# Optimization experiments

Measured on AMD Instinct MI355X. Metric: run time of the kernel, lower is better.

Reference implementation:

```python
import jax, jax.numpy as jnp
import numpy as np

N_NODES = 100000
N_FEAT = 512
HIDDEN = 64
N_CLASS = 40
N_EDGES = 3200000


def setup_inputs() -> dict:
    key = jax.random.key(0)
    k1, k2, k3, k4, k5, k6 = jax.random.split(key, 6)
    x = jax.random.normal(k1, (N_NODES, N_FEAT), dtype=jnp.float32)
    edge_index = jax.random.randint(k2, (2, N_EDGES), 0, N_NODES, dtype=jnp.int64)
    # Glorot-style init like PyG GCNConv
    s1 = (6.0 / (N_FEAT + HIDDEN)) ** 0.5
    s2 = (6.0 / (HIDDEN + N_CLASS)) ** 0.5
    W1 = jax.random.uniform(k3, (N_FEAT, HIDDEN), jnp.float32, -s1, s1)
    b1 = jnp.zeros((HIDDEN,), jnp.float32)
    W2 = jax.random.uniform(k4, (HIDDEN, N_CLASS), jnp.float32, -s2, s2)
    b2 = jnp.zeros((N_CLASS,), jnp.float32)
    return {"x": x, "edge_index": edge_index, "W1": W1, "b1": b1, "W2": W2, "b2": b2}


def _gcn_norm(edge_index, n_nodes):
    # add self-loops, symmetric normalization (PyG gcn_norm defaults)
    loops = jnp.arange(n_nodes, dtype=edge_index.dtype)
    src = jnp.concatenate([edge_index[0], loops])
    dst = jnp.concatenate([edge_index[1], loops])
    deg = jax.ops.segment_sum(jnp.ones_like(dst, dtype=jnp.float32), dst,
                              num_segments=n_nodes)
    dinv = jnp.where(deg > 0, jax.lax.rsqrt(deg), 0.0)
    norm = dinv[src] * dinv[dst]  # [E + N]
    return src, dst, norm


def _gcn_conv(h, src, dst, norm, W, b, n_nodes):
    h = h @ W                                   # [N, out]
    msg = h[src] * norm[:, None]                # gather + scale, [E+N, out]
    out = jax.ops.segment_sum(msg, dst, num_segments=n_nodes)  # scatter-add
    return out + b


def reference(x, edge_index, W1, b1, W2, b2):
    n = x.shape[0]
    src, dst, norm = _gcn_norm(edge_index, n)
    h = _gcn_conv(x, src, dst, norm, W1, b1, n)
    h = jax.nn.relu(h)
    h = _gcn_conv(h, src, dst, norm, W2, b2, n)
    return jax.nn.softmax(h, axis=-1)
```

## Files before the change

kernel.cpp:

```cpp
#include <hip/hip_runtime.h>
#include <hip/hip_bf16.h>
#include <math.h>

#define NFEAT 512
#define HID   64
#define NCLS  40
#define T2STRIDE 64

#define BSHIFT 9
#define BSIZE  512
#define BCAP   20480
#define CHUNK  4096

typedef __attribute__((ext_vector_type(8))) short bf16x8v;
typedef __attribute__((ext_vector_type(4))) float f32x4v;

__device__ __forceinline__ float rl_f(float v, int l) {
    return __int_as_float(__builtin_amdgcn_readlane(__float_as_int(v), l));
}
__device__ __forceinline__ unsigned short f2bf(float f) {
    __hip_bfloat16 h = __float2bfloat16(f);
    return *(unsigned short*)&h;
}


__global__ __launch_bounds__(256) void bin_scatter(const int* __restrict__ ei, int e,
                                                   int nbuckets,
                                                   int* __restrict__ bucket_cursor,
                                                   int* __restrict__ stage) {
    __shared__ int packed_s[CHUNK];
    __shared__ unsigned char bkt_s[CHUNK];
    __shared__ int hist[256];
    __shared__ int base_s[256];
    __shared__ int lcur[256];
    int t = threadIdx.x;
    int b0 = blockIdx.x * CHUNK;
    int cnt = min(CHUNK, e - b0);
    for (int i = t; i < 256; i += 256) hist[i] = 0;
    __syncthreads();
    for (int i = t; i < cnt; i += 256) {
        int s = ei[b0 + i];
        int d = ei[e + b0 + i];
        packed_s[i] = (s << BSHIFT) | (d & (BSIZE - 1));
        bkt_s[i] = (unsigned char)(d >> BSHIFT);
        atomicAdd(&hist[d >> BSHIFT], 1);
    }
    __syncthreads();
    for (int i = t; i < nbuckets; i += 256) {
        int c = hist[i];
        base_s[i] = c ? atomicAdd(&bucket_cursor[i], c) : 0;
        lcur[i] = 0;
    }
    __syncthreads();
    for (int i = t; i < cnt; i += 256) {
        int bk = bkt_s[i];
        int pos = base_s[bk] + atomicAdd(&lcur[bk], 1);
        if (pos < BCAP) stage[(size_t)bk * BCAP + pos] = packed_s[i];
    }
}

__global__ __launch_bounds__(256) void bucket_csr(const int* __restrict__ stage,
                                                  const int* __restrict__ bucket_cursor,
                                                  int* __restrict__ row_ptr,
                                                  float* __restrict__ dinv,
                                                  int* __restrict__ col,
                                                  int n, int e, int nbuckets) {
    __shared__ int sc[256];
    __shared__ int hist[BSIZE];
    __shared__ int lbase[BSIZE];
    __shared__ int psum[256];
    int b = blockIdx.x;
    int t = threadIdx.x;
    int v = (t < nbuckets) ? bucket_cursor[t] : 0;
    sc[t] = v;
    __syncthreads();
    #pragma unroll
    for (int off = 1; off < 256; off <<= 1) {
        int u = (t >= off) ? sc[t - off] : 0;
        __syncthreads();
        sc[t] += u;
        __syncthreads();
    }
    int base0 = (b > 0) ? sc[b - 1] : 0;
    if (b == 0 && t == 0) row_ptr[n] = e;

    int cnt = min(bucket_cursor[b], BCAP);
    int node0 = b << BSHIFT;
    int nnodes = min(BSIZE, n - node0);
    const int* st = stage + (size_t)b * BCAP;
    for (int i = t; i < BSIZE; i += 256) hist[i] = 0;
    __syncthreads();
    for (int i = t; i < cnt; i += 256) atomicAdd(&hist[st[i] & (BSIZE - 1)], 1);
    __syncthreads();
    int h0 = hist[2 * t], h1 = hist[2 * t + 1];
    int pair = h0 + h1;
    psum[t] = pair;
    __syncthreads();
    #pragma unroll
    for (int off = 1; off < 256; off <<= 1) {
        int u = (t >= off) ? psum[t - off] : 0;
        __syncthreads();
        psum[t] += u;
        __syncthreads();
    }
    int ex = psum[t] - pair;
    lbase[2 * t] = ex;
    lbase[2 * t + 1] = ex + h0;
    __syncthreads();
    for (int i = t; i < nnodes; i += 256) {
        row_ptr[node0 + i] = base0 + lbase[i];
        dinv[node0 + i] = rsqrtf((float)(hist[i] + 1));
    }
    __syncthreads();
    for (int i = t; i < cnt; i += 256) {
        int p = st[i];
        int pos = atomicAdd(&lbase[p & (BSIZE - 1)], 1);
        col[base0 + pos] = ((unsigned)p) >> BSHIFT;
    }
}


__global__ __launch_bounds__(256) void w1_to_bf16t(const float* __restrict__ W1,
                                                   unsigned short* __restrict__ w1bt) {
    int idx = blockIdx.x * 256 + threadIdx.x;
    int c = idx >> 9, k = idx & 511;
    w1bt[idx] = f2bf(W1[k * HID + c]);
}


__global__ __launch_bounds__(256) void gemm1(const float* __restrict__ x,
                                             const unsigned short* __restrict__ w1bt,
                                             const float* __restrict__ dinv,
                                             __hip_bfloat16* __restrict__ t1, int n) {
    __shared__ __align__(16) unsigned short As[64][40];
    __shared__ __align__(16) unsigned short Bs[64][40];
    int t = threadIdx.x;
    int m0 = blockIdx.x * 64;
    int w = t >> 6, lane = t & 63;
    int lrow = lane & 15, lkg = lane >> 4;
    f32x4v acc[4] = {};

    int arow = t >> 2;
    int akg = t & 3;
    int grow = m0 + arow; if (grow >= n) grow = n - 1;
    const float* xrow = x + (size_t)grow * NFEAT;

    for (int k0 = 0; k0 < NFEAT; k0 += 32) {
        float4 v0 = *(const float4*)(xrow + k0 + akg * 8);
        float4 v1 = *(const float4*)(xrow + k0 + akg * 8 + 4);
        union { unsigned short u[8]; uint4 q; } P;
        P.u[0] = f2bf(v0.x); P.u[1] = f2bf(v0.y); P.u[2] = f2bf(v0.z); P.u[3] = f2bf(v0.w);
        P.u[4] = f2bf(v1.x); P.u[5] = f2bf(v1.y); P.u[6] = f2bf(v1.z); P.u[7] = f2bf(v1.w);
        *(uint4*)&As[arow][akg * 8] = P.q;
        *(uint4*)&Bs[arow][akg * 8] = *(const uint4*)(w1bt + arow * 512 + k0 + akg * 8);
        __syncthreads();
        bf16x8v af = *(const bf16x8v*)&As[w * 16 + lrow][lkg * 8];
        #pragma unroll
        for (int nb = 0; nb < 4; nb++) {
            bf16x8v bfv = *(const bf16x8v*)&Bs[nb * 16 + lrow][lkg * 8];
            acc[nb] = __builtin_amdgcn_mfma_f32_16x16x32_bf16(af, bfv, acc[nb], 0, 0, 0);
        }
        __syncthreads();
    }
    #pragma unroll
    for (int r = 0; r < 4; r++) {
        int row = m0 + w * 16 + lkg * 4 + r;
        if (row < n) {
            float d = dinv[row];
            #pragma unroll
            for (int nb = 0; nb < 4; nb++) {
                t1[(size_t)row * HID + nb * 16 + lrow] = __float2bfloat16(acc[nb][r] * d);
            }
        }
    }
}


#define UNPACK_ADD(pv) do { \
    acc[0] += __uint_as_float((pv).x << 16); acc[1] += __uint_as_float((pv).x & 0xffff0000u); \
    acc[2] += __uint_as_float((pv).y << 16); acc[3] += __uint_as_float((pv).y & 0xffff0000u); \
    acc[4] += __uint_as_float((pv).z << 16); acc[5] += __uint_as_float((pv).z & 0xffff0000u); \
    acc[6] += __uint_as_float((pv).w << 16); acc[7] += __uint_as_float((pv).w & 0xffff0000u); } while (0)

__global__ __launch_bounds__(256) void agg1_gemm2(const __hip_bfloat16* __restrict__ t1,
                                                  const int* __restrict__ row_ptr,
                                                  const int* __restrict__ col,
                                                  const float* __restrict__ dinv,
                                                  const float* __restrict__ b1,
                                                  const float* __restrict__ W2,
                                                  __hip_bfloat16* __restrict__ t2, int n) {
    __shared__ float2 w2p[32 * 40];
    for (int i = threadIdx.x; i < 32 * 40; i += 256) {
        int k2 = i / 40, c = i - k2 * 40;
        w2p[i] = make_float2(W2[(2 * k2) * 40 + c], W2[(2 * k2 + 1) * 40 + c]);
    }
    __syncthreads();

    int wave = threadIdx.x >> 6;
    int lane = threadIdx.x & 63;
    int node0 = blockIdx.x * 4 + wave;
    int node = (node0 < n) ? node0 : n - 1;
    int r = lane & 7;
    int slot = lane >> 3;

    const uint4* t1q = (const uint4*)t1;
    int s0 = row_ptr[node], s1 = row_ptr[node + 1];

    float acc[8] = {0.f, 0.f, 0.f, 0.f, 0.f, 0.f, 0.f, 0.f};

    if (lane < 8) {
        uint4 pv = t1q[(size_t)node * 8 + lane];
        UNPACK_ADD(pv);
    }

    int bpbase = slot * 4;
    for (int jb = s0; jb < s1; jb += 32) {
        int rem = s1 - jb;
        int ll = lane & 31;
        int cidx = col[jb + ((ll < rem) ? ll : 0)];
        int srcg[4];
        #pragma unroll
        for (int g = 0; g < 4; g++) {
            int src = __builtin_amdgcn_ds_bpermute(bpbase + 32 * g, cidx);
            srcg[g] = (8 * g + slot < rem) ? src : n;
        }
        uint4 pv[4];
        #pragma unroll
        for (int g = 0; g < 4; g++) pv[g] = t1q[(size_t)srcg[g] * 8 + r];
        #pragma unroll
        for (int g = 0; g < 4; g++) { UNPACK_ADD(pv[g]); }
    }

    #pragma unroll
    for (int off = 8; off < 64; off <<= 1) {
        #pragma unroll
        for (int j = 0; j < 8; j++) acc[j] += __shfl_xor(acc[j], off, 64);
    }

    float dn = dinv[node];
    const float4* b1q = (const float4*)b1;
    float4 ba = b1q[2 * r];
    float4 bb = b1q[2 * r + 1];
    float hv[8];
    hv[0] = fmaxf(0.f, dn * acc[0] + ba.x);
    hv[1] = fmaxf(0.f, dn * acc[1] + ba.y);
    hv[2] = fmaxf(0.f, dn * acc[2] + ba.z);
    hv[3] = fmaxf(0.f, dn * acc[3] + ba.w);
    hv[4] = fmaxf(0.f, dn * acc[4] + bb.x);
    hv[5] = fmaxf(0.f, dn * acc[5] + bb.y);
    hv[6] = fmaxf(0.f, dn * acc[6] + bb.z);
    hv[7] = fmaxf(0.f, dn * acc[7] + bb.w);

    int c = (lane < 40) ? lane : 39;
    float o = 0.0f;
    #pragma unroll
    for (int rr = 0; rr < 8; rr++) {
        #pragma unroll
        for (int j2 = 0; j2 < 4; j2++) {
            float ha = rl_f(hv[2 * j2],     rr);
            float hb = rl_f(hv[2 * j2 + 1], rr);
            float2 wv = w2p[(4 * rr + j2) * 40 + c];
            o += ha * wv.x + hb * wv.y;
        }
    }
    if (node0 < n && lane < 40)
        t2[(size_t)node * T2STRIDE + lane] = __float2bfloat16(dn * o);
}


__global__ __launch_bounds__(256) void agg2_softmax(const __hip_bfloat16* __restrict__ t2,
                                                    const int* __restrict__ row_ptr,
                                                    const int* __restrict__ col,
                                                    const float* __restrict__ dinv,
                                                    const float* __restrict__ b2,
                                                    float* __restrict__ out, int n) {
    int wave = threadIdx.x >> 6;
    int lane = threadIdx.x & 63;
    int node = blockIdx.x * 4 + wave;
    if (node >= n) return;
    int h = lane >> 5;
    int p = lane & 31;
    int pc = (p < 20) ? p : 19;
    const unsigned* t2d = (const unsigned*)t2;
    int s0 = row_ptr[node], s1 = row_ptr[node + 1];

    float ax = 0.f, ay = 0.f;
    if (h == 0) {
        unsigned v = t2d[(size_t)node * 32 + pc];
        ax = __uint_as_float(v << 16);
        ay = __uint_as_float(v & 0xffff0000u);
    }
    for (int jb = s0; jb < s1; jb += 16) {
        int rem = s1 - jb;
        int cv = col[jb + ((lane < rem) ? lane : 0)];
        int srcg[8];
        #pragma unroll
        for (int i = 0; i < 8; i++) {
            int eid = 2 * i + h;
            int src = __builtin_amdgcn_ds_bpermute(4 * eid, cv);
            srcg[i] = (eid < rem) ? src : n;
        }
        unsigned pv[8];
        #pragma unroll
        for (int i = 0; i < 8; i++) pv[i] = t2d[(size_t)srcg[i] * 32 + pc];
        #pragma unroll
        for (int i = 0; i < 8; i++) {
            ax += __uint_as_float(pv[i] << 16);
            ay += __uint_as_float(pv[i] & 0xffff0000u);
        }
    }
    ax += __shfl_xor(ax, 32, 64);
    ay += __shfl_xor(ay, 32, 64);

    float dn = dinv[node];
    float2 bv = *(const float2*)(b2 + 2 * pc);
    float lx = dn * ax + bv.x;
    float ly = dn * ay + bv.y;
    float m = (p < 20) ? fmaxf(lx, ly) : -INFINITY;
    #pragma unroll
    for (int off = 16; off; off >>= 1) m = fmaxf(m, __shfl_xor(m, off, 64));
    float ex = (p < 20) ? expf(lx - m) : 0.0f;
    float ey = (p < 20) ? expf(ly - m) : 0.0f;
    float ssum = ex + ey;
    #pragma unroll
    for (int off = 16; off; off >>= 1) ssum += __shfl_xor(ssum, off, 64);
    if (h == 0 && p < 20) {
        *(float2*)(out + (size_t)node * NCLS + 2 * p) = make_float2(ex / ssum, ey / ssum);
    }
}


static inline size_t align256(size_t x) { return (x + 255) & ~(size_t)255; }

extern "C" void kernel_launch(void* const* d_in, const int* in_sizes, int n_in,
                              void* d_out, int out_size, void* d_ws, size_t ws_size,
                              hipStream_t stream) {
    const float* x  = (const float*)d_in[0];
    const int*   ei = (const int*)d_in[1];
    const float* W1 = (const float*)d_in[2];
    const float* b1 = (const float*)d_in[3];
    const float* W2 = (const float*)d_in[4];
    const float* b2 = (const float*)d_in[5];
    float* out = (float*)d_out;

    const int n = in_sizes[0] / NFEAT;
    const int e = in_sizes[1] / 2;
    const int nbuckets = (n + BSIZE - 1) >> BSHIFT;

    char* ws = (char*)d_ws;
    size_t off = 0;
    int*   row_ptr  = (int*)(ws + off);   off += align256((size_t)(n + 1) * 4);
    float* dinv     = (float*)(ws + off); off += align256((size_t)n * 4);
    int*   bcursor  = (int*)(ws + off);   off += align256(256 * 4);
    int*   col      = (int*)(ws + off);   off += align256((size_t)e * 4);
    int*   stage    = (int*)(ws + off);   off += align256((size_t)nbuckets * BCAP * 4);
    unsigned short* w1bt = (unsigned short*)(ws + off); off += align256((size_t)HID * NFEAT * 2);
    __hip_bfloat16* t1 = (__hip_bfloat16*)(ws + off); off += align256((size_t)(n + 1) * HID * 2);
    __hip_bfloat16* t2 = (__hip_bfloat16*)(ws + off); off += align256((size_t)(n + 1) * T2STRIDE * 2);

    (void)hipMemsetAsync(bcursor, 0, 256 * 4, stream);
    (void)hipMemsetAsync(t1 + (size_t)n * HID, 0, HID * 2, stream);
    (void)hipMemsetAsync(t2 + (size_t)n * T2STRIDE, 0, T2STRIDE * 2, stream);
    w1_to_bf16t<<<(HID * NFEAT) / 256, 256, 0, stream>>>(W1, w1bt);
    bin_scatter<<<(e + CHUNK - 1) / CHUNK, 256, 0, stream>>>(ei, e, nbuckets, bcursor, stage);
    bucket_csr<<<nbuckets, 256, 0, stream>>>(stage, bcursor, row_ptr, dinv, col, n, e, nbuckets);
    gemm1<<<(n + 63) / 64, 256, 0, stream>>>(x, w1bt, dinv, t1, n);
    agg1_gemm2<<<(n + 3) / 4, 256, 0, stream>>>(t1, row_ptr, col, dinv, b1, W2, t2, n);
    agg2_softmax<<<(n + 3) / 4, 256, 0, stream>>>(t2, row_ptr, col, dinv, b2, out, n);
}
```

Baseline: 550.8 us.

## Fuse memsets into prep kernel, widen CSR build blocks, add nontemporal loads

Replaces three hipMemsetAsync calls and the W1 transpose kernel with a single prep kernel that also zeroes the bucket cursors and padding rows. This removes several launch and memset overheads. It also doubles the block size of bin_scatter and bucket_csr to 512 threads, with a full 512-wide scan in bucket_csr. Nontemporal loads and stores are added for the edge index, the staging buffer, the x stream in gemm1 and the col reads in both aggregation kernels. The col reads in aggregation are reused by the second layer, so the nontemporal hints there could hurt cache reuse.

```diff
diff --git a/kernel.cpp b/kernel.cpp
--- a/kernel.cpp
+++ b/kernel.cpp
@@ -14,6 +14,7 @@
 
 typedef __attribute__((ext_vector_type(8))) short bf16x8v;
 typedef __attribute__((ext_vector_type(4))) float f32x4v;
+typedef __attribute__((ext_vector_type(4))) float v4f;
 
 __device__ __forceinline__ float rl_f(float v, int l) {
     return __int_as_float(__builtin_amdgcn_readlane(__float_as_int(v), l));
@@ -24,7 +25,23 @@
 }
 
 
-__global__ __launch_bounds__(256) void bin_scatter(const int* __restrict__ ei, int e,
+__global__ __launch_bounds__(256) void prep(const float* __restrict__ W1,
+                                            unsigned short* __restrict__ w1bt,
+                                            int* __restrict__ bcursor,
+                                            __hip_bfloat16* __restrict__ t1,
+                                            __hip_bfloat16* __restrict__ t2, int n) {
+    int idx = blockIdx.x * 256 + threadIdx.x;
+    int c = idx >> 9, k = idx & 511;
+    w1bt[idx] = f2bf(W1[k * HID + c]);
+    if (blockIdx.x == 0) bcursor[threadIdx.x] = 0;
+    if (blockIdx.x == 1 && threadIdx.x < 32)
+        ((unsigned*)(t1 + (size_t)n * HID))[threadIdx.x] = 0;
+    if (blockIdx.x == 2 && threadIdx.x < 32)
+        ((unsigned*)(t2 + (size_t)n * T2STRIDE))[threadIdx.x] = 0;
+}
+
+
+__global__ __launch_bounds__(512) void bin_scatter(const int* __restrict__ ei, int e,
                                                    int nbuckets,
                                                    int* __restrict__ bucket_cursor,
                                                    int* __restrict__ stage) {
@@ -36,30 +53,31 @@
     int t = threadIdx.x;
     int b0 = blockIdx.x * CHUNK;
     int cnt = min(CHUNK, e - b0);
-    for (int i = t; i < 256; i += 256) hist[i] = 0;
-    __syncthreads();
-    for (int i = t; i < cnt; i += 256) {
-        int s = ei[b0 + i];
-        int d = ei[e + b0 + i];
+    if (t < 256) hist[t] = 0;
+    __syncthreads();
+    for (int i = t; i < cnt; i += 512) {
+        int s = __builtin_nontemporal_load(ei + b0 + i);
+        int d = __builtin_nontemporal_load(ei + e + b0 + i);
         packed_s[i] = (s << BSHIFT) | (d & (BSIZE - 1));
         bkt_s[i] = (unsigned char)(d >> BSHIFT);
         atomicAdd(&hist[d >> BSHIFT], 1);
     }
     __syncthreads();
-    for (int i = t; i < nbuckets; i += 256) {
-        int c = hist[i];
-        base_s[i] = c ? atomicAdd(&bucket_cursor[i], c) : 0;
-        lcur[i] = 0;
-    }
-    __syncthreads();
-    for (int i = t; i < cnt; i += 256) {
+    if (t < 256) {
+        int c = (t < nbuckets) ? hist[t] : 0;
+        base_s[t] = c ? atomicAdd(&bucket_cursor[t], c) : 0;
+        lcur[t] = 0;
+    }
+    __syncthreads();
+    for (int i = t; i < cnt; i += 512) {
         int bk = bkt_s[i];
         int pos = base_s[bk] + atomicAdd(&lcur[bk], 1);
-        if (pos < BCAP) stage[(size_t)bk * BCAP + pos] = packed_s[i];
-    }
-}
-
-__global__ __launch_bounds__(256) void bucket_csr(const int* __restrict__ stage,
+        if (pos < BCAP) __builtin_nontemporal_store(packed_s[i], stage + (size_t)bk * BCAP + pos);
+    }
+}
+
+
+__global__ __launch_bounds__(512) void bucket_csr(const int* __restrict__ stage,
                                                   const int* __restrict__ bucket_cursor,
                                                   int* __restrict__ row_ptr,
                                                   float* __restrict__ dinv,
@@ -68,17 +86,16 @@
     __shared__ int sc[256];
     __shared__ int hist[BSIZE];
     __shared__ int lbase[BSIZE];
-    __shared__ int psum[256];
+    __shared__ int psum[BSIZE];
     int b = blockIdx.x;
     int t = threadIdx.x;
-    int v = (t < nbuckets) ? bucket_cursor[t] : 0;
-    sc[t] = v;
+    if (t < 256) sc[t] = (t < nbuckets) ? bucket_cursor[t] : 0;
     __syncthreads();
     #pragma unroll
     for (int off = 1; off < 256; off <<= 1) {
-        int u = (t >= off) ? sc[t - off] : 0;
-        __syncthreads();
-        sc[t] += u;
+        int u = (t < 256 && t >= off) ? sc[t - off] : 0;
+        __syncthreads();
+        if (t < 256) sc[t] += u;
         __syncthreads();
     }
     int base0 = (b > 0) ? sc[b - 1] : 0;
@@ -88,43 +105,33 @@
     int node0 = b << BSHIFT;
     int nnodes = min(BSIZE, n - node0);
     const int* st = stage + (size_t)b * BCAP;
-    for (int i = t; i < BSIZE; i += 256) hist[i] = 0;
-    __syncthreads();
-    for (int i = t; i < cnt; i += 256) atomicAdd(&hist[st[i] & (BSIZE - 1)], 1);
-    __syncthreads();
-    int h0 = hist[2 * t], h1 = hist[2 * t + 1];
-    int pair = h0 + h1;
-    psum[t] = pair;
-    __syncthreads();
-    #pragma unroll
-    for (int off = 1; off < 256; off <<= 1) {
+    hist[t] = 0;
+    __syncthreads();
+    for (int i = t; i < cnt; i += 512)
+        atomicAdd(&hist[__builtin_nontemporal_load(st + i) & (BSIZE - 1)], 1);
+    __syncthreads();
+    int d = hist[t];
+    psum[t] = d;
+    __syncthreads();
+    #pragma unroll
+    for (int off = 1; off < 512; off <<= 1) {
         int u = (t >= off) ? psum[t - off] : 0;
         __syncthreads();
         psum[t] += u;
         __syncthreads();
     }
-    int ex = psum[t] - pair;
-    lbase[2 * t] = ex;
-    lbase[2 * t + 1] = ex + h0;
-    __syncthreads();
-    for (int i = t; i < nnodes; i += 256) {
-        row_ptr[node0 + i] = base0 + lbase[i];
-        dinv[node0 + i] = rsqrtf((float)(hist[i] + 1));
-    }
-    __syncthreads();
-    for (int i = t; i < cnt; i += 256) {
-        int p = st[i];
+    int myl = psum[t] - d;
+    lbase[t] = myl;
+    if (t < nnodes) {
+        row_ptr[node0 + t] = base0 + myl;
+        dinv[node0 + t] = rsqrtf((float)(d + 1));
+    }
+    __syncthreads();
+    for (int i = t; i < cnt; i += 512) {
+        int p = __builtin_nontemporal_load(st + i);
         int pos = atomicAdd(&lbase[p & (BSIZE - 1)], 1);
         col[base0 + pos] = ((unsigned)p) >> BSHIFT;
     }
-}
-
-
-__global__ __launch_bounds__(256) void w1_to_bf16t(const float* __restrict__ W1,
-                                                   unsigned short* __restrict__ w1bt) {
-    int idx = blockIdx.x * 256 + threadIdx.x;
-    int c = idx >> 9, k = idx & 511;
-    w1bt[idx] = f2bf(W1[k * HID + c]);
 }
 
 
@@ -146,8 +153,8 @@
     const float* xrow = x + (size_t)grow * NFEAT;
 
     for (int k0 = 0; k0 < NFEAT; k0 += 32) {
-        float4 v0 = *(const float4*)(xrow + k0 + akg * 8);
-        float4 v1 = *(const float4*)(xrow + k0 + akg * 8 + 4);
+        v4f v0 = __builtin_nontemporal_load((const v4f*)(xrow + k0 + akg * 8));
+        v4f v1 = __builtin_nontemporal_load((const v4f*)(xrow + k0 + akg * 8 + 4));
         union { unsigned short u[8]; uint4 q; } P;
         P.u[0] = f2bf(v0.x); P.u[1] = f2bf(v0.y); P.u[2] = f2bf(v0.z); P.u[3] = f2bf(v0.w);
         P.u[4] = f2bf(v1.x); P.u[5] = f2bf(v1.y); P.u[6] = f2bf(v1.z); P.u[7] = f2bf(v1.w);
@@ -217,7 +224,7 @@
     for (int jb = s0; jb < s1; jb += 32) {
         int rem = s1 - jb;
         int ll = lane & 31;
-        int cidx = col[jb + ((ll < rem) ? ll : 0)];
+        int cidx = __builtin_nontemporal_load(col + jb + ((ll < rem) ? ll : 0));
         int srcg[4];
         #pragma unroll
         for (int g = 0; g < 4; g++) {
@@ -292,7 +299,7 @@
     }
     for (int jb = s0; jb < s1; jb += 16) {
         int rem = s1 - jb;
-        int cv = col[jb + ((lane < rem) ? lane : 0)];
+        int cv = __builtin_nontemporal_load(col + jb + ((lane < rem) ? lane : 0));
         int srcg[8];
         #pragma unroll
         for (int i = 0; i < 8; i++) {
@@ -358,12 +365,9 @@
     __hip_bfloat16* t1 = (__hip_bfloat16*)(ws + off); off += align256((size_t)(n + 1) * HID * 2);
     __hip_bfloat16* t2 = (__hip_bfloat16*)(ws + off); off += align256((size_t)(n + 1) * T2STRIDE * 2);
 
-    (void)hipMemsetAsync(bcursor, 0, 256 * 4, stream);
-    (void)hipMemsetAsync(t1 + (size_t)n * HID, 0, HID * 2, stream);
-    (void)hipMemsetAsync(t2 + (size_t)n * T2STRIDE, 0, T2STRIDE * 2, stream);
-    w1_to_bf16t<<<(HID * NFEAT) / 256, 256, 0, stream>>>(W1, w1bt);
-    bin_scatter<<<(e + CHUNK - 1) / CHUNK, 256, 0, stream>>>(ei, e, nbuckets, bcursor, stage);
-    bucket_csr<<<nbuckets, 256, 0, stream>>>(stage, bcursor, row_ptr, dinv, col, n, e, nbuckets);
+    prep<<<(HID * NFEAT) / 256, 256, 0, stream>>>(W1, w1bt, bcursor, t1, t2, n);
+    bin_scatter<<<(e + CHUNK - 1) / CHUNK, 512, 0, stream>>>(ei, e, nbuckets, bcursor, stage);
+    bucket_csr<<<nbuckets, 512, 0, stream>>>(stage, bcursor, row_ptr, dinv, col, n, e, nbuckets);
     gemm1<<<(n + 63) / 64, 256, 0, stream>>>(x, w1bt, dinv, t1, n);
     agg1_gemm2<<<(n + 3) / 4, 256, 0, stream>>>(t1, row_ptr, col, dinv, b1, W2, t2, n);
     agg2_softmax<<<(n + 3) / 4, 256, 0, stream>>>(t2, row_ptr, col, dinv, b2, out, n);
```

New measurement: 634.3 us. 15.2% more time.
